# Performance work log

Hardware: AMD Instinct MI355X
Metric: run time of the kernel (lower is better)

The kernel has to match this reference:

```python
import jax, jax.numpy as jnp
import numpy as np

D_MODEL = 512
NUM_HEADS = 8
DEPTH = D_MODEL // NUM_HEADS


def setup_inputs() -> dict:
    key = jax.random.key(0)
    kx, kq, kk, kv, ko = jax.random.split(key, 5)
    scale = 1.0 / np.sqrt(D_MODEL)
    return {
        "x": jax.random.normal(kx, (4, 2048, D_MODEL), dtype=jnp.float32),
        "W_q": jax.random.normal(kq, (D_MODEL, D_MODEL), dtype=jnp.float32) * scale,
        "W_k": jax.random.normal(kk, (D_MODEL, D_MODEL), dtype=jnp.float32) * scale,
        "W_v": jax.random.normal(kv, (D_MODEL, D_MODEL), dtype=jnp.float32) * scale,
        "W_o": jax.random.normal(ko, (D_MODEL, D_MODEL), dtype=jnp.float32) * scale,
    }


def reference(x, W_q, W_k, W_v, W_o):
    B, S, _ = x.shape
    # nn.Linear with weight W: y = x @ W.T
    def split_heads(t):
        return t.reshape(B, S, NUM_HEADS, DEPTH).transpose(0, 2, 1, 3)  # [B,H,S,D]
    Q = split_heads(x @ W_q.T)
    K = split_heads(x @ W_k.T)
    V = split_heads(x @ W_v.T)
    b = -jnp.log(jnp.asarray(S, dtype=jnp.float32))  # -log(seq_len) bias
    inv_sqrt_dk = 1.0 / jnp.sqrt(jnp.asarray(DEPTH, dtype=jnp.float32))
    qk = jnp.einsum('bhqd,bhkd->bhqk', Q, K) * inv_sqrt_dk
    attn = jax.nn.sigmoid(qk + b)  # non-softmax sigmoid attention
    out = jnp.einsum('bhqk,bhkd->bhqd', attn, V)
    out = out.transpose(0, 2, 1, 3).reshape(B, S, D_MODEL)
    return out @ W_o.T
```

## Files before the change

### kernel.cpp

```cpp
#include <hip/hip_runtime.h>
#include <stdint.h>

typedef _Float16 f16x8 __attribute__((ext_vector_type(8)));
typedef _Float16 f16x4 __attribute__((ext_vector_type(4)));
typedef __fp16 h16x2 __attribute__((ext_vector_type(2)));
typedef float f32x4 __attribute__((ext_vector_type(4)));
typedef float f32x16 __attribute__((ext_vector_type(16)));

#define SEQ 2048
#define NHEADS 8

#define GLOAD_LDS16(gp, lp)                                                        \
  __builtin_amdgcn_global_load_lds(                                                \
      (const __attribute__((address_space(1))) void*)(uintptr_t)(const void*)(gp), \
      (__attribute__((address_space(3))) void*)(uintptr_t)(void*)(lp), 16, 0, 0)

__device__ __forceinline__ void barrier_lds() {
  __builtin_amdgcn_s_waitcnt(0xc07f);
  __builtin_amdgcn_s_barrier();
}

__device__ __forceinline__ f16x4 pack4(float a, float b, float c, float d) {
  h16x2 lo = __builtin_amdgcn_cvt_pkrtz(a, b);
  h16x2 hi = __builtin_amdgcn_cvt_pkrtz(c, d);
  f16x4 o;
  o.x = (_Float16)lo.x; o.y = (_Float16)lo.y;
  o.z = (_Float16)hi.x; o.w = (_Float16)hi.y;
  return o;
}

__global__ void cvt_all_kernel(const float* __restrict__ x, const float* __restrict__ wq,
                               const float* __restrict__ wk, const float* __restrict__ wv,
                               const float* __restrict__ wo, _Float16* __restrict__ xh,
                               _Float16* __restrict__ wh) {
  int i = blockIdx.x * 256 + threadIdx.x;
  const float* src;
  _Float16* dst;
  int off;
  if (i < 1048576) {
    src = x; dst = xh; off = i;
  } else {
    int j = i - 1048576;
    int sel = j >> 16;
    off = j & 65535;
    src = (sel == 0) ? wq : (sel == 1) ? wk : (sel == 2) ? wv : wo;
    dst = wh + (size_t)sel * 262144;
  }
  float4 v = ((const float4*)src)[off];
  ((f16x4*)dst)[off] = pack4(v.x, v.y, v.z, v.w);
}

__device__ __forceinline__ void gemm_tile_bt(const _Float16* __restrict__ A,
                                             const _Float16* __restrict__ B,
                                             int m0, int n0,
                                             _Float16* lds,
                                             f32x4 (&acc)[4][4]) {
  const int tid = threadIdx.x;
  const int w = tid >> 6, lane = tid & 63;
  const int wr = w >> 1, wc = w & 1;
  const int lrow = lane & 15, q = lane >> 4;
  const int snb = w * 32 + (lane >> 3);
  const int scb = lane & 7;

#pragma unroll
  for (int i = 0; i < 4; ++i)
#pragma unroll
    for (int j = 0; j < 4; ++j)
#pragma unroll
      for (int r = 0; r < 4; ++r) acc[i][j][r] = 0.f;

#pragma unroll
  for (int t = 0; t < 4; ++t) {
    int n = snb + t * 8;
    int cbg = scb ^ (n & 7);
    GLOAD_LDS16(A + (size_t)(m0 + n) * 512 + cbg * 8, lds + (w * 32 + t * 8) * 64);
    GLOAD_LDS16(B + (size_t)(n0 + n) * 512 + cbg * 8, lds + 8192 + (w * 32 + t * 8) * 64);
  }

  for (int kt = 0; kt < 8; ++kt) {
    __syncthreads();
    if (kt < 7) {
      _Float16* nb = lds + ((kt + 1) & 1) * 16384;
#pragma unroll
      for (int t = 0; t < 4; ++t) {
        int n = snb + t * 8;
        int cbg = scb ^ (n & 7);
        GLOAD_LDS16(A + (size_t)(m0 + n) * 512 + (kt + 1) * 64 + cbg * 8, nb + (w * 32 + t * 8) * 64);
        GLOAD_LDS16(B + (size_t)(n0 + n) * 512 + (kt + 1) * 64 + cbg * 8, nb + 8192 + (w * 32 + t * 8) * 64);
      }
    }
    _Float16* As = lds + (kt & 1) * 16384;
    _Float16* Bs = As + 8192;

    f16x8 af[4][2], bfr[4][2];
#pragma unroll
    for (int i = 0; i < 4; ++i) {
      int m = wr * 64 + i * 16 + lrow;
#pragma unroll
      for (int kk = 0; kk < 2; ++kk) {
        int cb = (kk * 4 + q) ^ (m & 7);
        af[i][kk] = *(const f16x8*)(As + m * 64 + cb * 8);
      }
    }
#pragma unroll
    for (int j = 0; j < 4; ++j) {
      int n = wc * 64 + j * 16 + lrow;
#pragma unroll
      for (int kk = 0; kk < 2; ++kk) {
        int cb = (kk * 4 + q) ^ (n & 7);
        bfr[j][kk] = *(const f16x8*)(Bs + n * 64 + cb * 8);
      }
    }
#pragma unroll
    for (int i = 0; i < 4; ++i)
#pragma unroll
      for (int j = 0; j < 4; ++j) {
        acc[i][j] = __builtin_amdgcn_mfma_f32_16x16x32_f16(af[i][0], bfr[j][0], acc[i][j], 0, 0, 0);
        acc[i][j] = __builtin_amdgcn_mfma_f32_16x16x32_f16(af[i][1], bfr[j][1], acc[i][j], 0, 0, 0);
      }
  }
}

__global__ __launch_bounds__(256, 2) void qkv_kernel(
    const _Float16* __restrict__ xb, const _Float16* __restrict__ Wq,
    const _Float16* __restrict__ Wk, const _Float16* __restrict__ Wv,
    _Float16* __restrict__ Qo, _Float16* __restrict__ Ko, _Float16* __restrict__ Vto) {
  __shared__ _Float16 pool[32768];
  const int z = blockIdx.z;
  f32x4 acc[4][4];
  const int tid = threadIdx.x, w = tid >> 6, lane = tid & 63;
  const int wr = w >> 1, wc = w & 1, lcol = lane & 15, q = lane >> 4;

  if (z < 2) {
    const int m0 = blockIdx.y * 128;
    const int n0 = blockIdx.x * 128;
    gemm_tile_bt((z == 0) ? Wq : Wk, xb, m0, n0, pool, acc);
    _Float16* outp = (z == 0) ? Qo : Ko;
    __syncthreads();
#pragma unroll
    for (int i = 0; i < 4; ++i) {
      int cl = wr * 64 + i * 16 + q * 4;
#pragma unroll
      for (int j = 0; j < 4; ++j) {
        int s = wc * 64 + j * 16 + lcol;
        *(f16x4*)(pool + s * 136 + cl) =
            pack4(acc[i][j][0], acc[i][j][1], acc[i][j][2], acc[i][j][3]);
      }
    }
    __syncthreads();
#pragma unroll
    for (int it = 0; it < 16; ++it) {
      int srow = it * 8 + (tid >> 5);
      int ch = tid & 31;
      f16x4 v = *(const f16x4*)(pool + srow * 136 + ch * 4);
      *(f16x4*)(outp + (size_t)(n0 + srow) * 512 + m0 + ch * 4) = v;
    }
  } else {
    const int m0 = blockIdx.x * 128;
    const int n0 = blockIdx.y * 128;
    gemm_tile_bt(xb, Wv, m0, n0, pool, acc);
    const int bb = m0 >> 11, sl0 = m0 & 2047;
    __syncthreads();
#pragma unroll
    for (int i = 0; i < 4; ++i) {
      int s0 = wr * 64 + i * 16 + q * 4;
#pragma unroll
      for (int j = 0; j < 4; ++j) {
        int c = wc * 64 + j * 16 + lcol;
        *(f16x4*)(pool + c * 136 + s0) =
            pack4(acc[i][j][0], acc[i][j][1], acc[i][j][2], acc[i][j][3]);
      }
    }
    __syncthreads();
#pragma unroll
    for (int it = 0; it < 16; ++it) {
      int crow = it * 8 + (tid >> 5);
      int ch = tid & 31;
      int cg = n0 + crow, h = cg >> 6, d = cg & 63;
      f16x4 v = *(const f16x4*)(pool + crow * 136 + ch * 4);
      *(f16x4*)(Vto + ((size_t)((bb * NHEADS + h) * 64 + d)) * SEQ + sl0 + ch * 4) = v;
    }
  }
}

__device__ __forceinline__ void load_win(const _Float16* Ksc, const _Float16* Vtsc,
                                         int m, int klp, int fk, int fq,
                                         int hi, int q31,
                                         f16x8 (&ka)[4], f16x8 (&vb)[2][2]) {
  const int krow = m * 32 + klp;
#pragma unroll
  for (int s = 0; s < 4; ++s) {
    int cb = (s * 2 + hi) ^ fk;
    ka[s] = *(const f16x8*)(Ksc + krow * 64 + cb * 8);
  }
#pragma unroll
  for (int ww = 0; ww < 2; ++ww)
#pragma unroll
    for (int t = 0; t < 2; ++t) {
      int drow = t * 32 + q31;
      int g = m * 4 + ww * 2 + hi;
      int cb = g ^ fq;
      vb[ww][t] = *(const f16x8*)(Vtsc + drow * 64 + cb * 8);
    }
}

__device__ __forceinline__ void attn_window(const f16x8 (&ka)[4], const f16x8 (&vb)[2][2],
                                            const f16x8 (&qb)[4], const f32x16& z16,
                                            f32x16& o0, f32x16& o1) {
  const float c1 = 0.18033688011112042f;
  __builtin_amdgcn_s_setprio(1);
  f32x16 sacc = __builtin_amdgcn_mfma_f32_32x32x16_f16(ka[0], qb[0], z16, 0, 0, 0);
  sacc = __builtin_amdgcn_mfma_f32_32x32x16_f16(ka[1], qb[1], sacc, 0, 0, 0);
  sacc = __builtin_amdgcn_mfma_f32_32x32x16_f16(ka[2], qb[2], sacc, 0, 0, 0);
  sacc = __builtin_amdgcn_mfma_f32_32x32x16_f16(ka[3], qb[3], sacc, 0, 0, 0);
  __builtin_amdgcn_s_setprio(0);

  float p[16];
#pragma unroll
  for (int r = 0; r < 16; ++r) {
    float wp = __builtin_amdgcn_exp2f(__builtin_fmaf(sacc[r], c1, -1.0f));
    float e = wp * 0.0009765625f;
    p[r] = __builtin_fmaf(wp, __builtin_fmaf(e, e, -e), wp);
  }

  f16x8 pa[2];
#pragma unroll
  for (int ww = 0; ww < 2; ++ww) {
    h16x2 a0 = __builtin_amdgcn_cvt_pkrtz(p[8 * ww + 0], p[8 * ww + 1]);
    h16x2 a1 = __builtin_amdgcn_cvt_pkrtz(p[8 * ww + 2], p[8 * ww + 3]);
    h16x2 a2 = __builtin_amdgcn_cvt_pkrtz(p[8 * ww + 4], p[8 * ww + 5]);
    h16x2 a3 = __builtin_amdgcn_cvt_pkrtz(p[8 * ww + 6], p[8 * ww + 7]);
    pa[ww][0] = (_Float16)a0.x; pa[ww][1] = (_Float16)a0.y;
    pa[ww][2] = (_Float16)a1.x; pa[ww][3] = (_Float16)a1.y;
    pa[ww][4] = (_Float16)a2.x; pa[ww][5] = (_Float16)a2.y;
    pa[ww][6] = (_Float16)a3.x; pa[ww][7] = (_Float16)a3.y;
  }

  __builtin_amdgcn_s_setprio(1);
  o0 = __builtin_amdgcn_mfma_f32_32x32x16_f16(pa[0], vb[0][0], o0, 0, 0, 0);
  o1 = __builtin_amdgcn_mfma_f32_32x32x16_f16(pa[0], vb[0][1], o1, 0, 0, 0);
  o0 = __builtin_amdgcn_mfma_f32_32x32x16_f16(pa[1], vb[1][0], o0, 0, 0, 0);
  o1 = __builtin_amdgcn_mfma_f32_32x32x16_f16(pa[1], vb[1][1], o1, 0, 0, 0);
  __builtin_amdgcn_s_setprio(0);
}

__global__ __launch_bounds__(256, 4) void attn_kernel(
    const _Float16* __restrict__ Qw, const _Float16* __restrict__ Kw,
    const _Float16* __restrict__ Vtw, _Float16* __restrict__ Ow,
    _Float16* __restrict__ Op) {
  __shared__ _Float16 lds[16384];

  const int tid = threadIdx.x, w = tid >> 6, lane = tid & 63;
  const int q31 = lane & 31, hi = lane >> 5;

  const int L = blockIdx.x;
  const int xcd = L & 7, slot = L >> 3;
  const int bh = xcd * 4 + (slot >> 5);
  const int rem = slot & 31;
  const int qt = rem >> 1, ks = rem & 1;
  const int b = bh >> 3, h = bh & 7;
  const int q0 = qt * 128;

  const _Float16* Qp = Qw + ((size_t)(b * SEQ + q0)) * 512 + h * 64;
  const _Float16* Kp = Kw + ((size_t)b * SEQ) * 512 + h * 64 + (size_t)ks * 1024 * 512;
  const _Float16* Vp = Vtw + (size_t)bh * 64 * SEQ + (size_t)ks * 1024;

  const int l3 = lane >> 3, l7 = lane & 7;

  int koff[2], voff[2];
#pragma unroll
  for (int t = 0; t < 2; ++t) {
    int n = w * 16 + t * 8 + l3;
    int cbg = l7 ^ l3 ^ ((t & 1) << 2);
    koff[t] = n * 1024 + cbg * 16;
    voff[t] = n * 4096 + cbg * 16;
  }
  const char* kgb = (const char*)Kp;
  const char* vgb = (const char*)Vp;

  _Float16* Qs = lds + 8192;
#pragma unroll
  for (int t = 0; t < 4; ++t) {
    int n = w * 32 + t * 8 + l3;
    int cbg = l7 ^ l3 ^ ((t & 1) << 2);
    GLOAD_LDS16((const char*)Qp + n * 1024 + cbg * 16, Qs + (w * 32 + t * 8) * 64);
  }
#pragma unroll
  for (int t = 0; t < 2; ++t) {
    GLOAD_LDS16(kgb + koff[t], lds + (w * 16 + t * 8) * 64);
    GLOAD_LDS16(vgb + voff[t], lds + 4096 + (w * 16 + t * 8) * 64);
  }
  kgb += 65536;
  vgb += 128;
  __syncthreads();

  const int fq = (q31 & 7) ^ (((q31 >> 3) & 1) << 2);
  const int klp = (q31 & 3) | ((q31 & 4) << 1) | ((q31 & 8) >> 1) | (q31 & 16);
  const int fk = (klp & 7) ^ (((klp >> 3) & 1) << 2);

  f16x8 qb[4];
  const int qrow = w * 32 + q31;
#pragma unroll
  for (int s = 0; s < 4; ++s) {
    int cb = (s * 2 + hi) ^ fq;
    qb[s] = *(const f16x8*)(Qs + qrow * 64 + cb * 8);
  }

  f32x16 oacc[2];
  f32x16 z16;
#pragma unroll
  for (int r = 0; r < 16; ++r) { z16[r] = 0.f; oacc[0][r] = 0.f; oacc[1][r] = 0.f; }

  for (int kt = 0; kt < 16; ++kt) {
    __syncthreads();
    if (kt < 15) {
      _Float16* nb = lds + ((kt + 1) & 1) * 8192;
#pragma unroll
      for (int t = 0; t < 2; ++t) {
        GLOAD_LDS16(kgb + koff[t], nb + (w * 16 + t * 8) * 64);
        GLOAD_LDS16(vgb + voff[t], nb + 4096 + (w * 16 + t * 8) * 64);
      }
      kgb += 65536;
      vgb += 128;
    }
    const _Float16* Ksc = lds + (kt & 1) * 8192;
    const _Float16* Vtsc = Ksc + 4096;

    f16x8 ka0[4], ka1[4], vb0[2][2], vb1[2][2];
    load_win(Ksc, Vtsc, 0, klp, fk, fq, hi, q31, ka0, vb0);
    attn_window(ka0, vb0, qb, z16, oacc[0], oacc[1]);
    load_win(Ksc, Vtsc, 1, klp, fk, fq, hi, q31, ka1, vb1);
    attn_window(ka1, vb1, qb, z16, oacc[0], oacc[1]);
  }

  barrier_lds();
  _Float16* Ob = lds;
  _Float16* outp = ks ? Op : Ow;
#pragma unroll
  for (int t = 0; t < 2; ++t) {
#pragma unroll
    for (int r = 0; r < 16; ++r) {
      int row = w * 32 + (r & 3) + ((r >> 2) << 3) + hi * 4;
      int d = t * 32 + q31;
      Ob[row * 72 + d] = (_Float16)(oacc[t][r] * 0.0009765625f);
    }
  }
  barrier_lds();
#pragma unroll
  for (int it = 0; it < 8; ++it) {
    int row = it * 16 + (tid >> 4);
    int ch = tid & 15;
    f16x4 v = *(const f16x4*)(Ob + row * 72 + ch * 4);
    *(f16x4*)(outp + (size_t)(b * SEQ + q0 + row) * 512 + h * 64 + ch * 4) = v;
  }
}

__global__ void combine_kernel(_Float16* __restrict__ o, const _Float16* __restrict__ p) {
  int i = blockIdx.x * 256 + threadIdx.x;
  f16x8 a = ((const f16x8*)o)[i];
  f16x8 c = ((const f16x8*)p)[i];
  ((f16x8*)o)[i] = a + c;
}

__global__ __launch_bounds__(256, 2) void oproj_kernel(
    const _Float16* __restrict__ A, const _Float16* __restrict__ Wo,
    float* __restrict__ out) {
  __shared__ _Float16 pool[32768];
  const int m0 = blockIdx.x * 128, n0 = blockIdx.y * 128;
  f32x4 acc[4][4];
  gemm_tile_bt(A, Wo, m0, n0, pool, acc);

  const int tid = threadIdx.x, w = tid >> 6, lane = tid & 63;
  const int wr = w >> 1, wc = w & 1, lcol = lane & 15, q = lane >> 4;
#pragma unroll
  for (int i = 0; i < 4; ++i) {
    int gm0 = m0 + wr * 64 + i * 16 + q * 4;
#pragma unroll
    for (int j = 0; j < 4; ++j) {
      int gn = n0 + wc * 64 + j * 16 + lcol;
#pragma unroll
      for (int r = 0; r < 4; ++r)
        out[(size_t)(gm0 + r) * 512 + gn] = acc[i][j][r];
    }
  }
}

extern "C" void kernel_launch(void* const* d_in, const int* in_sizes, int n_in,
                              void* d_out, int out_size, void* d_ws, size_t ws_size,
                              hipStream_t stream) {
  const float* x = (const float*)d_in[0];
  const float* Wq = (const float*)d_in[1];
  const float* Wk = (const float*)d_in[2];
  const float* Wv = (const float*)d_in[3];
  const float* Wo = (const float*)d_in[4];
  float* out = (float*)d_out;
  char* ws = (char*)d_ws;

  _Float16* xh = (_Float16*)(ws + 0);
  _Float16* wh = (_Float16*)(ws + 8388608);
  _Float16* Qw = (_Float16*)(ws + 10485760);
  _Float16* Kw = (_Float16*)(ws + 18874368);
  _Float16* Vtw = (_Float16*)(ws + 27262976);
  _Float16* Ow = (_Float16*)(ws + 35651584);

  _Float16* wqh = wh;
  _Float16* wkh = wh + 262144;
  _Float16* wvh = wh + 524288;
  _Float16* woh = wh + 786432;

  cvt_all_kernel<<<5120, 256, 0, stream>>>(x, Wq, Wk, Wv, Wo, xh, wh);
  qkv_kernel<<<dim3(64, 4, 3), 256, 0, stream>>>(xh, wqh, wkh, wvh, Qw, Kw, Vtw);
  attn_kernel<<<1024, 256, 0, stream>>>(Qw, Kw, Vtw, Ow, xh);
  combine_kernel<<<2048, 256, 0, stream>>>(Ow, xh);
  oproj_kernel<<<dim3(64, 4), 256, 0, stream>>>(Ow, woh, out);
}
```

Measured before the change: 161.9 us.

## Drop key-split in attention, remove combine kernel, hand-schedule LDS reads

The attention kernel no longer splits the key sequence across two blocks. Each of 512 blocks now walks all 2048 keys, so the separate combine kernel and its partial-output round trip through memory go away. The inner loop is unrolled by two over the double buffer and uses inline-asm ds_read_b128 with immediate offsets and explicit lgkmcnt waits, so the second window's reads overlap the first window's compute. Launch bounds drop to 2 blocks per SM. The cost is half the grid parallelism and longer serial chains per block, which may underfill the GPU.

```diff
diff --git a/kernel.cpp b/kernel.cpp
--- a/kernel.cpp
+++ b/kernel.cpp
@@ -14,6 +14,15 @@
   __builtin_amdgcn_global_load_lds(                                                \
       (const __attribute__((address_space(1))) void*)(uintptr_t)(const void*)(gp), \
       (__attribute__((address_space(3))) void*)(uintptr_t)(void*)(lp), 16, 0, 0)
+
+#define DSR(dst, base, off) \
+  asm volatile("ds_read_b128 %0, %1 offset:%c2" : "=v"(dst) : "v"(base), "i"(off))
+
+#define WAIT_LGKM(n)                                         \
+  do {                                                       \
+    asm volatile("s_waitcnt lgkmcnt(%c0)" ::"i"(n) : "memory"); \
+    __builtin_amdgcn_sched_barrier(0);                       \
+  } while (0)
 
 __device__ __forceinline__ void barrier_lds() {
   __builtin_amdgcn_s_waitcnt(0xc07f);
@@ -183,71 +192,93 @@
   }
 }
 
-__device__ __forceinline__ void load_win(const _Float16* Ksc, const _Float16* Vtsc,
-                                         int m, int klp, int fk, int fq,
-                                         int hi, int q31,
-                                         f16x8 (&ka)[4], f16x8 (&vb)[2][2]) {
-  const int krow = m * 32 + klp;
-#pragma unroll
-  for (int s = 0; s < 4; ++s) {
-    int cb = (s * 2 + hi) ^ fk;
-    ka[s] = *(const f16x8*)(Ksc + krow * 64 + cb * 8);
-  }
-#pragma unroll
-  for (int ww = 0; ww < 2; ++ww)
-#pragma unroll
-    for (int t = 0; t < 2; ++t) {
-      int drow = t * 32 + q31;
-      int g = m * 4 + ww * 2 + hi;
-      int cb = g ^ fq;
-      vb[ww][t] = *(const f16x8*)(Vtsc + drow * 64 + cb * 8);
-    }
-}
-
-__device__ __forceinline__ void attn_window(const f16x8 (&ka)[4], const f16x8 (&vb)[2][2],
-                                            const f16x8 (&qb)[4], const f32x16& z16,
-                                            f32x16& o0, f32x16& o1) {
+__device__ __forceinline__ void attn_window(
+    f16x8 k0, f16x8 k1, f16x8 k2, f16x8 k3,
+    f16x8 v00, f16x8 v01, f16x8 v10, f16x8 v11,
+    const f16x8 (&qb)[4], const f32x16& z16, f32x16& o0, f32x16& o1) {
   const float c1 = 0.18033688011112042f;
   __builtin_amdgcn_s_setprio(1);
-  f32x16 sacc = __builtin_amdgcn_mfma_f32_32x32x16_f16(ka[0], qb[0], z16, 0, 0, 0);
-  sacc = __builtin_amdgcn_mfma_f32_32x32x16_f16(ka[1], qb[1], sacc, 0, 0, 0);
-  sacc = __builtin_amdgcn_mfma_f32_32x32x16_f16(ka[2], qb[2], sacc, 0, 0, 0);
-  sacc = __builtin_amdgcn_mfma_f32_32x32x16_f16(ka[3], qb[3], sacc, 0, 0, 0);
+  f32x16 s = __builtin_amdgcn_mfma_f32_32x32x16_f16(k0, qb[0], z16, 0, 0, 0);
+  s = __builtin_amdgcn_mfma_f32_32x32x16_f16(k1, qb[1], s, 0, 0, 0);
+  s = __builtin_amdgcn_mfma_f32_32x32x16_f16(k2, qb[2], s, 0, 0, 0);
+  s = __builtin_amdgcn_mfma_f32_32x32x16_f16(k3, qb[3], s, 0, 0, 0);
   __builtin_amdgcn_s_setprio(0);
 
   float p[16];
 #pragma unroll
   for (int r = 0; r < 16; ++r) {
-    float wp = __builtin_amdgcn_exp2f(__builtin_fmaf(sacc[r], c1, -1.0f));
+    float wp = __builtin_amdgcn_exp2f(__builtin_fmaf(s[r], c1, -1.0f));
     float e = wp * 0.0009765625f;
     p[r] = __builtin_fmaf(wp, __builtin_fmaf(e, e, -e), wp);
   }
 
-  f16x8 pa[2];
-#pragma unroll
-  for (int ww = 0; ww < 2; ++ww) {
-    h16x2 a0 = __builtin_amdgcn_cvt_pkrtz(p[8 * ww + 0], p[8 * ww + 1]);
-    h16x2 a1 = __builtin_amdgcn_cvt_pkrtz(p[8 * ww + 2], p[8 * ww + 3]);
-    h16x2 a2 = __builtin_amdgcn_cvt_pkrtz(p[8 * ww + 4], p[8 * ww + 5]);
-    h16x2 a3 = __builtin_amdgcn_cvt_pkrtz(p[8 * ww + 6], p[8 * ww + 7]);
-    pa[ww][0] = (_Float16)a0.x; pa[ww][1] = (_Float16)a0.y;
-    pa[ww][2] = (_Float16)a1.x; pa[ww][3] = (_Float16)a1.y;
-    pa[ww][4] = (_Float16)a2.x; pa[ww][5] = (_Float16)a2.y;
-    pa[ww][6] = (_Float16)a3.x; pa[ww][7] = (_Float16)a3.y;
+  f16x8 pa0, pa1;
+  {
+    h16x2 a0 = __builtin_amdgcn_cvt_pkrtz(p[0], p[1]);
+    h16x2 a1 = __builtin_amdgcn_cvt_pkrtz(p[2], p[3]);
+    h16x2 a2 = __builtin_amdgcn_cvt_pkrtz(p[4], p[5]);
+    h16x2 a3 = __builtin_amdgcn_cvt_pkrtz(p[6], p[7]);
+    pa0[0] = (_Float16)a0.x; pa0[1] = (_Float16)a0.y;
+    pa0[2] = (_Float16)a1.x; pa0[3] = (_Float16)a1.y;
+    pa0[4] = (_Float16)a2.x; pa0[5] = (_Float16)a2.y;
+    pa0[6] = (_Float16)a3.x; pa0[7] = (_Float16)a3.y;
+    h16x2 b0 = __builtin_amdgcn_cvt_pkrtz(p[8], p[9]);
+    h16x2 b1 = __builtin_amdgcn_cvt_pkrtz(p[10], p[11]);
+    h16x2 b2 = __builtin_amdgcn_cvt_pkrtz(p[12], p[13]);
+    h16x2 b3 = __builtin_amdgcn_cvt_pkrtz(p[14], p[15]);
+    pa1[0] = (_Float16)b0.x; pa1[1] = (_Float16)b0.y;
+    pa1[2] = (_Float16)b1.x; pa1[3] = (_Float16)b1.y;
+    pa1[4] = (_Float16)b2.x; pa1[5] = (_Float16)b2.y;
+    pa1[6] = (_Float16)b3.x; pa1[7] = (_Float16)b3.y;
   }
 
   __builtin_amdgcn_s_setprio(1);
-  o0 = __builtin_amdgcn_mfma_f32_32x32x16_f16(pa[0], vb[0][0], o0, 0, 0, 0);
-  o1 = __builtin_amdgcn_mfma_f32_32x32x16_f16(pa[0], vb[0][1], o1, 0, 0, 0);
-  o0 = __builtin_amdgcn_mfma_f32_32x32x16_f16(pa[1], vb[1][0], o0, 0, 0, 0);
-  o1 = __builtin_amdgcn_mfma_f32_32x32x16_f16(pa[1], vb[1][1], o1, 0, 0, 0);
+  o0 = __builtin_amdgcn_mfma_f32_32x32x16_f16(pa0, v00, o0, 0, 0, 0);
+  o1 = __builtin_amdgcn_mfma_f32_32x32x16_f16(pa0, v01, o1, 0, 0, 0);
+  o0 = __builtin_amdgcn_mfma_f32_32x32x16_f16(pa1, v10, o0, 0, 0, 0);
+  o1 = __builtin_amdgcn_mfma_f32_32x32x16_f16(pa1, v11, o1, 0, 0, 0);
   __builtin_amdgcn_s_setprio(0);
 }
 
-__global__ __launch_bounds__(256, 4) void attn_kernel(
+#define KT_BODY(BUFB, NBUFB, PF)                                              \
+  {                                                                           \
+    __syncthreads();                                                          \
+    if (PF) {                                                                 \
+      _Float16* nb = (_Float16*)((char*)lds + (NBUFB));                       \
+      GLOAD_LDS16(kgb + koff[0], nb + (w * 16) * 64);                         \
+      GLOAD_LDS16(kgb + koff[1], nb + (w * 16 + 8) * 64);                     \
+      GLOAD_LDS16(vgb + voff[0], nb + 4096 + (w * 16) * 64);                  \
+      GLOAD_LDS16(vgb + voff[1], nb + 4096 + (w * 16 + 8) * 64);              \
+      kgb += 65536;                                                           \
+      vgb += 128;                                                             \
+    }                                                                         \
+    f16x8 kA0, kA1, kA2, kA3, vA00, vA01, vA10, vA11;                         \
+    f16x8 kB0, kB1, kB2, kB3, vB00, vB01, vB10, vB11;                         \
+    DSR(kA0, kb0, (BUFB));                                                    \
+    DSR(kA1, kb1, (BUFB));                                                    \
+    DSR(kA2, kb2, (BUFB));                                                    \
+    DSR(kA3, kb3, (BUFB));                                                    \
+    DSR(vA00, pv00, (BUFB) + 8192);                                           \
+    DSR(vA01, pv00, (BUFB) + 12288);                                          \
+    DSR(vA10, pv01, (BUFB) + 8192);                                           \
+    DSR(vA11, pv01, (BUFB) + 12288);                                          \
+    DSR(kB0, kb0, (BUFB) + 4096);                                             \
+    DSR(kB1, kb1, (BUFB) + 4096);                                             \
+    DSR(kB2, kb2, (BUFB) + 4096);                                             \
+    DSR(kB3, kb3, (BUFB) + 4096);                                             \
+    DSR(vB00, pv10, (BUFB) + 8192);                                           \
+    DSR(vB01, pv10, (BUFB) + 12288);                                          \
+    DSR(vB10, pv11, (BUFB) + 8192);                                           \
+    DSR(vB11, pv11, (BUFB) + 12288);                                          \
+    WAIT_LGKM(8);                                                             \
+    attn_window(kA0, kA1, kA2, kA3, vA00, vA01, vA10, vA11, qb, z16, oacc0, oacc1); \
+    WAIT_LGKM(0);                                                             \
+    attn_window(kB0, kB1, kB2, kB3, vB00, vB01, vB10, vB11, qb, z16, oacc0, oacc1); \
+  }
+
+__global__ __launch_bounds__(256, 2) void attn_kernel(
     const _Float16* __restrict__ Qw, const _Float16* __restrict__ Kw,
-    const _Float16* __restrict__ Vtw, _Float16* __restrict__ Ow,
-    _Float16* __restrict__ Op) {
+    const _Float16* __restrict__ Vtw, _Float16* __restrict__ Ow) {
   __shared__ _Float16 lds[16384];
 
   const int tid = threadIdx.x, w = tid >> 6, lane = tid & 63;
@@ -255,15 +286,13 @@
 
   const int L = blockIdx.x;
   const int xcd = L & 7, slot = L >> 3;
-  const int bh = xcd * 4 + (slot >> 5);
-  const int rem = slot & 31;
-  const int qt = rem >> 1, ks = rem & 1;
+  const int bh = xcd * 4 + (slot >> 4), qt = slot & 15;
   const int b = bh >> 3, h = bh & 7;
   const int q0 = qt * 128;
 
   const _Float16* Qp = Qw + ((size_t)(b * SEQ + q0)) * 512 + h * 64;
-  const _Float16* Kp = Kw + ((size_t)b * SEQ) * 512 + h * 64 + (size_t)ks * 1024 * 512;
-  const _Float16* Vp = Vtw + (size_t)bh * 64 * SEQ + (size_t)ks * 1024;
+  const _Float16* Kp = Kw + ((size_t)b * SEQ) * 512 + h * 64;
+  const _Float16* Vp = Vtw + (size_t)bh * 64 * SEQ;
 
   const int l3 = lane >> 3, l7 = lane & 7;
 
@@ -285,11 +314,10 @@
     int cbg = l7 ^ l3 ^ ((t & 1) << 2);
     GLOAD_LDS16((const char*)Qp + n * 1024 + cbg * 16, Qs + (w * 32 + t * 8) * 64);
   }
-#pragma unroll
-  for (int t = 0; t < 2; ++t) {
-    GLOAD_LDS16(kgb + koff[t], lds + (w * 16 + t * 8) * 64);
-    GLOAD_LDS16(vgb + voff[t], lds + 4096 + (w * 16 + t * 8) * 64);
-  }
+  GLOAD_LDS16(kgb + koff[0], lds + (w * 16) * 64);
+  GLOAD_LDS16(kgb + koff[1], lds + (w * 16 + 8) * 64);
+  GLOAD_LDS16(vgb + voff[0], lds + 4096 + (w * 16) * 64);
+  GLOAD_LDS16(vgb + voff[1], lds + 4096 + (w * 16 + 8) * 64);
   kgb += 65536;
   vgb += 128;
   __syncthreads();
@@ -306,43 +334,34 @@
     qb[s] = *(const f16x8*)(Qs + qrow * 64 + cb * 8);
   }
 
-  f32x16 oacc[2];
-  f32x16 z16;
-#pragma unroll
-  for (int r = 0; r < 16; ++r) { z16[r] = 0.f; oacc[0][r] = 0.f; oacc[1][r] = 0.f; }
-
-  for (int kt = 0; kt < 16; ++kt) {
-    __syncthreads();
-    if (kt < 15) {
-      _Float16* nb = lds + ((kt + 1) & 1) * 8192;
-#pragma unroll
-      for (int t = 0; t < 2; ++t) {
-        GLOAD_LDS16(kgb + koff[t], nb + (w * 16 + t * 8) * 64);
-        GLOAD_LDS16(vgb + voff[t], nb + 4096 + (w * 16 + t * 8) * 64);
-      }
-      kgb += 65536;
-      vgb += 128;
-    }
-    const _Float16* Ksc = lds + (kt & 1) * 8192;
-    const _Float16* Vtsc = Ksc + 4096;
-
-    f16x8 ka0[4], ka1[4], vb0[2][2], vb1[2][2];
-    load_win(Ksc, Vtsc, 0, klp, fk, fq, hi, q31, ka0, vb0);
-    attn_window(ka0, vb0, qb, z16, oacc[0], oacc[1]);
-    load_win(Ksc, Vtsc, 1, klp, fk, fq, hi, q31, ka1, vb1);
-    attn_window(ka1, vb1, qb, z16, oacc[0], oacc[1]);
+  const int kb0 = klp * 128 + (((0 * 2 + hi) ^ fk) << 4);
+  const int kb1 = klp * 128 + (((1 * 2 + hi) ^ fk) << 4);
+  const int kb2 = klp * 128 + (((2 * 2 + hi) ^ fk) << 4);
+  const int kb3 = klp * 128 + (((3 * 2 + hi) ^ fk) << 4);
+  const int pv00 = q31 * 128 + (((0 + 0 + hi) ^ fq) << 4);
+  const int pv01 = q31 * 128 + (((0 + 2 + hi) ^ fq) << 4);
+  const int pv10 = q31 * 128 + (((4 + 0 + hi) ^ fq) << 4);
+  const int pv11 = q31 * 128 + (((4 + 2 + hi) ^ fq) << 4);
+
+  f32x16 oacc0, oacc1, z16;
+#pragma unroll
+  for (int r = 0; r < 16; ++r) { z16[r] = 0.f; oacc0[r] = 0.f; oacc1[r] = 0.f; }
+
+  for (int p = 0; p < 16; ++p) {
+    KT_BODY(0, 16384, true);
+    KT_BODY(16384, 0, (p < 15));
   }
 
   barrier_lds();
   _Float16* Ob = lds;
-  _Float16* outp = ks ? Op : Ow;
 #pragma unroll
   for (int t = 0; t < 2; ++t) {
 #pragma unroll
     for (int r = 0; r < 16; ++r) {
       int row = w * 32 + (r & 3) + ((r >> 2) << 3) + hi * 4;
       int d = t * 32 + q31;
-      Ob[row * 72 + d] = (_Float16)(oacc[t][r] * 0.0009765625f);
+      float v = (t == 0) ? oacc0[r] : oacc1[r];
+      Ob[row * 72 + d] = (_Float16)(v * 0.0009765625f);
     }
   }
   barrier_lds();
@@ -351,15 +370,8 @@
     int row = it * 16 + (tid >> 4);
     int ch = tid & 15;
     f16x4 v = *(const f16x4*)(Ob + row * 72 + ch * 4);
-    *(f16x4*)(outp + (size_t)(b * SEQ + q0 + row) * 512 + h * 64 + ch * 4) = v;
-  }
-}
-
-__global__ void combine_kernel(_Float16* __restrict__ o, const _Float16* __restrict__ p) {
-  int i = blockIdx.x * 256 + threadIdx.x;
-  f16x8 a = ((const f16x8*)o)[i];
-  f16x8 c = ((const f16x8*)p)[i];
-  ((f16x8*)o)[i] = a + c;
+    *(f16x4*)(Ow + (size_t)(b * SEQ + q0 + row) * 512 + h * 64 + ch * 4) = v;
+  }
 }
 
 __global__ __launch_bounds__(256, 2) void oproj_kernel(
@@ -410,7 +422,6 @@
 
   cvt_all_kernel<<<5120, 256, 0, stream>>>(x, Wq, Wk, Wv, Wo, xh, wh);
   qkv_kernel<<<dim3(64, 4, 3), 256, 0, stream>>>(xh, wqh, wkh, wvh, Qw, Kw, Vtw);
-  attn_kernel<<<1024, 256, 0, stream>>>(Qw, Kw, Vtw, Ow, xh);
-  combine_kernel<<<2048, 256, 0, stream>>>(Ow, xh);
+  attn_kernel<<<512, 256, 0, stream>>>(Qw, Kw, Vtw, Ow);
   oproj_kernel<<<dim3(64, 4), 256, 0, stream>>>(Ow, woh, out);
 }
```

New measurement: 149.8 us. -7.5%, faster.
